# Kernel optimization log

Hardware: AMD Instinct MI355X
Metric: run time of the kernel (lower is better)

## Reference

```python
import jax, jax.numpy as jnp
import numpy as np

TAU = 0.5  # init tau
EPS = 1e-8  # F.cosine_similarity eps


def setup_inputs() -> dict:
    key = jax.random.key(0)
    k1, k2 = jax.random.split(key)
    N, D, NUM_CLASSES = 4096, 1024, 128
    layer_embeds = jax.random.normal(k1, (N, D), dtype=jnp.float32)
    y_true = jax.random.randint(k2, (N,), 0, NUM_CLASSES, dtype=jnp.int64)
    return {"layer_embeds": layer_embeds, "y_true": y_true}


def reference(layer_embeds, y_true):
    N = layer_embeds.shape[0]
    # batched cosine similarity, scaled like the original: (cos + 1) * 0.5 * tau
    norms = jnp.maximum(jnp.linalg.norm(layer_embeds, axis=1), EPS)  # [N]
    cos = (layer_embeds @ layer_embeds.T) / (norms[:, None] * norms[None, :])  # [N, N]
    S = (cos + 1.0) * 0.5 * TAU

    same = y_true[:, None] == y_true[None, :]  # [N, N]
    eye = jnp.eye(N, dtype=bool)
    pos_mask = same & ~eye            # same-label pairs, j != i
    neg_mask = ~same                  # different-label pairs (diag excluded since same there)

    # column 0: first positive (in j order), else stays 0
    has_pos = pos_mask.any(axis=1)
    first_pos = jnp.argmax(pos_mask, axis=1)
    pos_val = jnp.where(has_pos, S[jnp.arange(N), first_pos], 0.0)  # [N]

    # negatives fill columns 1.. in j order: col = 1 + (#negatives with j' < j)
    negi = neg_mask.astype(jnp.int32)
    col = 1 + jnp.cumsum(negi, axis=1) - negi  # [N, N]
    W = 2 * N  # pad one dummy column for non-negative entries
    cols = jnp.where(neg_mask, col, W - 1)
    rows = jnp.broadcast_to(jnp.arange(N)[:, None], (N, N))
    loss_temp = jnp.zeros((N, W), dtype=jnp.float32)
    loss_temp = loss_temp.at[rows, cols].set(jnp.where(neg_mask, S, 0.0))
    loss_temp = loss_temp.at[:, 0].set(pos_val)
    loss_temp = loss_temp[:, : 2 * N - 1]  # [N, 2N-1], matches torch buffer

    # -log_softmax, take column 0, sum over rows, divide by N
    lse = jax.nn.logsumexp(loss_temp, axis=1)  # [N]
    loss = jnp.sum(lse - loss_temp[:, 0]) / N
    return loss
```

## Files before the change

### kernel.cpp

```cpp
#include <hip/hip_runtime.h>
#include <hip/hip_bf16.h>
#include <math.h>

#define NN 4096
#define DD 1024
#define NCLS 128
#define TAU 0.5f
#define EPSV 1e-8f

typedef __bf16 bf16;
typedef __bf16 bf16x8 __attribute__((ext_vector_type(8)));
typedef __bf16 bf16x4 __attribute__((ext_vector_type(4)));
typedef float f32x4 __attribute__((ext_vector_type(4)));

__device__ __forceinline__ void gl2lds16(const void* g, void* l) {
    __builtin_amdgcn_global_load_lds(
        (const __attribute__((address_space(1))) void*)g,
        (__attribute__((address_space(3))) void*)l,
        16, 0, 0);
}

__global__ __launch_bounds__(256) void k_norm_cast(const float* __restrict__ X,
                                                   bf16* __restrict__ Xn,
                                                   float* __restrict__ rsum) {
    int w = threadIdx.x >> 6, lane = threadIdx.x & 63;
    int row = blockIdx.x * 4 + w;
    const float* xr = X + (size_t)row * DD;
    float4 v[4];
    float ss = 0.f;
#pragma unroll
    for (int c = 0; c < 4; ++c) {
        v[c] = *(const float4*)(xr + c * 256 + lane * 4);
        ss += v[c].x * v[c].x + v[c].y * v[c].y + v[c].z * v[c].z + v[c].w * v[c].w;
    }
#pragma unroll
    for (int m = 1; m < 64; m <<= 1) ss += __shfl_xor(ss, m, 64);
    float rn = 1.f / fmaxf(sqrtf(ss), EPSV);
    if (lane == 0) rsum[row] = 0.f;
#pragma unroll
    for (int c = 0; c < 4; ++c) {
        bf16x4 o;
        o.x = (bf16)(v[c].x * rn);
        o.y = (bf16)(v[c].y * rn);
        o.z = (bf16)(v[c].z * rn);
        o.w = (bf16)(v[c].w * rn);
        *(bf16x4*)(Xn + (size_t)row * DD + c * 256 + lane * 4) = o;
    }
}

__global__ __launch_bounds__(1024) void k_classes(const int* __restrict__ y,
                                                  int* __restrict__ cnt,
                                                  int* __restrict__ mn1,
                                                  int* __restrict__ mn2,
                                                  float* __restrict__ out) {
    __shared__ int sc[NCLS], s1[NCLS], s2[NCLS];
    int t = threadIdx.x;
    if (t < NCLS) { sc[t] = 0; s1[t] = 0x7fffffff; s2[t] = 0x7fffffff; }
    __syncthreads();
    int yv[4];
#pragma unroll
    for (int k = 0; k < 4; ++k) {
        int i = t + k * 1024;
        yv[k] = y[i];
        atomicAdd(&sc[yv[k]], 1);
        atomicMin(&s1[yv[k]], i);
    }
    __syncthreads();
#pragma unroll
    for (int k = 0; k < 4; ++k) {
        int i = t + k * 1024;
        if (s1[yv[k]] != i) atomicMin(&s2[yv[k]], i);
    }
    __syncthreads();
    if (t < NCLS) { cnt[t] = sc[t]; mn1[t] = s1[t]; mn2[t] = s2[t]; }
    if (t == 0) out[0] = 0.f;
}

__global__ __launch_bounds__(256) void k_gemm(const bf16* __restrict__ Xn,
                                              const int* __restrict__ y,
                                              float* __restrict__ rowsum) {
    __shared__ __align__(16) bf16 As[128 * 32];
    __shared__ __align__(16) bf16 Bs[128 * 32];
    __shared__ int yA[128], yB[128];

    int id = blockIdx.x;
    float ff = sqrtf((float)(8 * id + 1));
    int bj = (int)((ff - 1.f) * 0.5f);
    if (bj * (bj + 1) / 2 > id) bj--;
    if ((bj + 1) * (bj + 2) / 2 <= id) bj++;
    int bi = id - bj * (bj + 1) / 2;
    const int rowA0 = bi * 128;
    const int rowB0 = bj * 128;
    const bool diag = (bi == bj);

    const int tid = threadIdx.x;
    if (tid < 128) yA[tid] = y[rowA0 + tid];
    else           yB[tid - 128] = y[rowB0 + tid - 128];

    const int lane = tid & 63;
    const int w = tid >> 6;
    const int wm = w & 1, wn = w >> 1;
    const int lr = lane >> 4, lc = lane & 15;

    f32x4 acc[4][4];
#pragma unroll
    for (int i = 0; i < 4; ++i)
#pragma unroll
        for (int j = 0; j < 4; ++j) acc[i][j] = (f32x4){0.f, 0.f, 0.f, 0.f};

    const int r = tid >> 2;
    const int g = tid & 3;
    const int kg = g ^ ((r >> 1) & 3);
    const bf16* gA0 = Xn + (size_t)(rowA0 + r) * DD + kg * 8;
    const bf16* gA1 = gA0 + (size_t)64 * DD;
    const bf16* gB0 = Xn + (size_t)(rowB0 + r) * DD + kg * 8;
    const bf16* gB1 = gB0 + (size_t)64 * DD;
    bf16* lA0 = As + tid * 8;
    bf16* lA1 = As + 64 * 32 + tid * 8;
    bf16* lB0 = Bs + tid * 8;
    bf16* lB1 = Bs + 64 * 32 + tid * 8;

    const int sw = (lc >> 1) & 3;

    for (int k0 = 0; k0 < DD; k0 += 32) {
        __syncthreads();
        gl2lds16(gA0 + k0, lA0);
        gl2lds16(gA1 + k0, lA1);
        gl2lds16(gB0 + k0, lB0);
        gl2lds16(gB1 + k0, lB1);
        __syncthreads();

        bf16x8 af[4], bfr[4];
#pragma unroll
        for (int mt = 0; mt < 4; ++mt)
            af[mt] = *(const bf16x8*)(As + (wm * 64 + mt * 16 + lc) * 32 + ((lr ^ sw) * 8));
#pragma unroll
        for (int nt = 0; nt < 4; ++nt)
            bfr[nt] = *(const bf16x8*)(Bs + (wn * 64 + nt * 16 + lc) * 32 + ((lr ^ sw) * 8));
#pragma unroll
        for (int mt = 0; mt < 4; ++mt)
#pragma unroll
            for (int nt = 0; nt < 4; ++nt)
                acc[mt][nt] = __builtin_amdgcn_mfma_f32_16x16x32_bf16(
                    af[mt], bfr[nt], acc[mt][nt], 0, 0, 0);
    }

    int ycol[4];
#pragma unroll
    for (int nt = 0; nt < 4; ++nt) ycol[nt] = yB[wn * 64 + nt * 16 + lc];
    float colacc[4] = {0.f, 0.f, 0.f, 0.f};
#pragma unroll
    for (int mt = 0; mt < 4; ++mt) {
#pragma unroll
        for (int rr = 0; rr < 4; ++rr) {
            int rloc = wm * 64 + mt * 16 + lr * 4 + rr;
            int yrow = yA[rloc];
            float s = 0.f;
#pragma unroll
            for (int nt = 0; nt < 4; ++nt) {
                float Sv = (acc[mt][nt][rr] + 1.f) * (0.5f * TAU);
                float e = (ycol[nt] != yrow) ? __expf(Sv) : 0.f;
                s += e;
                colacc[nt] += e;
            }
            s += __shfl_xor(s, 1, 16);
            s += __shfl_xor(s, 2, 16);
            s += __shfl_xor(s, 4, 16);
            s += __shfl_xor(s, 8, 16);
            if (lc == 0) atomicAdd(&rowsum[rowA0 + rloc], s);
        }
    }
    if (!diag) {
#pragma unroll
        for (int nt = 0; nt < 4; ++nt) {
            float cs = colacc[nt];
            cs += __shfl_xor(cs, 16, 64);
            cs += __shfl_xor(cs, 32, 64);
            if (lane < 16) atomicAdd(&rowsum[rowB0 + wn * 64 + nt * 16 + lane], cs);
        }
    }
}

__global__ __launch_bounds__(256) void k_tail(const bf16* __restrict__ Xn,
                                              const int* __restrict__ y,
                                              const int* __restrict__ cnt,
                                              const int* __restrict__ mn1,
                                              const int* __restrict__ mn2,
                                              const float* __restrict__ rowsum,
                                              float* __restrict__ out) {
    int w = threadIdx.x >> 6, lane = threadIdx.x & 63;
    int i = blockIdx.x * 4 + w;
    int c = y[i];
    int cc = cnt[c];
    float pv = 0.f;
    if (cc >= 2) {
        int fp = (mn1[c] == i) ? mn2[c] : mn1[c];
        const bf16* xi = Xn + (size_t)i * DD;
        const bf16* xf = Xn + (size_t)fp * DD;
        float dot = 0.f;
#pragma unroll
        for (int q = 0; q < 2; ++q) {
            bf16x8 a = *(const bf16x8*)(xi + q * 512 + lane * 8);
            bf16x8 b = *(const bf16x8*)(xf + q * 512 + lane * 8);
#pragma unroll
            for (int e = 0; e < 8; ++e) dot += (float)a[e] * (float)b[e];
        }
#pragma unroll
        for (int m = 1; m < 64; m <<= 1) dot += __shfl_xor(dot, m, 64);
        pv = (dot + 1.f) * (0.5f * TAU);
    }
    float contrib = logf(rowsum[i] + __expf(pv) + (float)(NN - 2 + cc)) - pv;
    __shared__ float wsum[4];
    if (lane == 0) wsum[w] = contrib;
    __syncthreads();
    if (threadIdx.x == 0)
        atomicAdd(out, (wsum[0] + wsum[1] + wsum[2] + wsum[3]) * (1.f / (float)NN));
}

extern "C" void kernel_launch(void* const* d_in, const int* in_sizes, int n_in,
                              void* d_out, int out_size, void* d_ws, size_t ws_size,
                              hipStream_t stream) {
    const float* X = (const float*)d_in[0];
    const int* y = (const int*)d_in[1];
    float* out = (float*)d_out;

    char* ws = (char*)d_ws;
    bf16* Xn    = (bf16*)ws;
    float* rsum = (float*)(ws + 8 * 1024 * 1024);
    int* cnt    = (int*)(ws + 8 * 1024 * 1024 + 16 * 1024);
    int* mn1    = (int*)(ws + 8 * 1024 * 1024 + 16 * 1024 + 512);
    int* mn2    = (int*)(ws + 8 * 1024 * 1024 + 16 * 1024 + 1024);

    k_norm_cast<<<dim3(NN / 4), 256, 0, stream>>>(X, Xn, rsum);
    k_classes<<<dim3(1), 1024, 0, stream>>>(y, cnt, mn1, mn2, out);
    k_gemm<<<dim3(528), 256, 0, stream>>>(Xn, y, rsum);
    k_tail<<<dim3(NN / 4), 256, 0, stream>>>(Xn, y, cnt, mn1, mn2, rsum, out);
}
```

Measured before the change: 115.7 us.

## Double-buffer GEMM LDS tiles and fuse norm and class-stat kernels

New measurement: 119.9 us. 1.04x slower.

```diff
diff --git a/kernel.cpp b/kernel.cpp
--- a/kernel.cpp
+++ b/kernel.cpp
@@ -20,67 +20,68 @@
         16, 0, 0);
 }
 
-__global__ __launch_bounds__(256) void k_norm_cast(const float* __restrict__ X,
-                                                   bf16* __restrict__ Xn,
-                                                   float* __restrict__ rsum) {
-    int w = threadIdx.x >> 6, lane = threadIdx.x & 63;
-    int row = blockIdx.x * 4 + w;
-    const float* xr = X + (size_t)row * DD;
-    float4 v[4];
-    float ss = 0.f;
-#pragma unroll
-    for (int c = 0; c < 4; ++c) {
-        v[c] = *(const float4*)(xr + c * 256 + lane * 4);
-        ss += v[c].x * v[c].x + v[c].y * v[c].y + v[c].z * v[c].z + v[c].w * v[c].w;
-    }
-#pragma unroll
-    for (int m = 1; m < 64; m <<= 1) ss += __shfl_xor(ss, m, 64);
-    float rn = 1.f / fmaxf(sqrtf(ss), EPSV);
-    if (lane == 0) rsum[row] = 0.f;
-#pragma unroll
-    for (int c = 0; c < 4; ++c) {
-        bf16x4 o;
-        o.x = (bf16)(v[c].x * rn);
-        o.y = (bf16)(v[c].y * rn);
-        o.z = (bf16)(v[c].z * rn);
-        o.w = (bf16)(v[c].w * rn);
-        *(bf16x4*)(Xn + (size_t)row * DD + c * 256 + lane * 4) = o;
-    }
-}
-
-__global__ __launch_bounds__(1024) void k_classes(const int* __restrict__ y,
-                                                  int* __restrict__ cnt,
-                                                  int* __restrict__ mn1,
-                                                  int* __restrict__ mn2,
-                                                  float* __restrict__ out) {
-    __shared__ int sc[NCLS], s1[NCLS], s2[NCLS];
-    int t = threadIdx.x;
-    if (t < NCLS) { sc[t] = 0; s1[t] = 0x7fffffff; s2[t] = 0x7fffffff; }
-    __syncthreads();
-    int yv[4];
-#pragma unroll
-    for (int k = 0; k < 4; ++k) {
-        int i = t + k * 1024;
-        yv[k] = y[i];
-        atomicAdd(&sc[yv[k]], 1);
-        atomicMin(&s1[yv[k]], i);
-    }
-    __syncthreads();
-#pragma unroll
-    for (int k = 0; k < 4; ++k) {
-        int i = t + k * 1024;
-        if (s1[yv[k]] != i) atomicMin(&s2[yv[k]], i);
-    }
-    __syncthreads();
-    if (t < NCLS) { cnt[t] = sc[t]; mn1[t] = s1[t]; mn2[t] = s2[t]; }
-    if (t == 0) out[0] = 0.f;
+__global__ __launch_bounds__(256) void k_prep(const float* __restrict__ X,
+                                              bf16* __restrict__ Xn,
+                                              float* __restrict__ rsum,
+                                              const int* __restrict__ y,
+                                              int* __restrict__ cnt,
+                                              int* __restrict__ mn1,
+                                              int* __restrict__ mn2,
+                                              float* __restrict__ out) {
+    if (blockIdx.x < 1024) {
+        int w = threadIdx.x >> 6, lane = threadIdx.x & 63;
+        int row = blockIdx.x * 4 + w;
+        const float* xr = X + (size_t)row * DD;
+        float4 v[4];
+        float ss = 0.f;
+#pragma unroll
+        for (int c = 0; c < 4; ++c) {
+            v[c] = *(const float4*)(xr + c * 256 + lane * 4);
+            ss += v[c].x * v[c].x + v[c].y * v[c].y + v[c].z * v[c].z + v[c].w * v[c].w;
+        }
+#pragma unroll
+        for (int m = 1; m < 64; m <<= 1) ss += __shfl_xor(ss, m, 64);
+        float rn = 1.f / fmaxf(sqrtf(ss), EPSV);
+        if (lane == 0) rsum[row] = 0.f;
+#pragma unroll
+        for (int c = 0; c < 4; ++c) {
+            bf16x4 o;
+            o.x = (bf16)(v[c].x * rn);
+            o.y = (bf16)(v[c].y * rn);
+            o.z = (bf16)(v[c].z * rn);
+            o.w = (bf16)(v[c].w * rn);
+            *(bf16x4*)(Xn + (size_t)row * DD + c * 256 + lane * 4) = o;
+        }
+    } else {
+        __shared__ int sc[NCLS], s1[NCLS], s2[NCLS];
+        int t = threadIdx.x;
+        if (t < NCLS) { sc[t] = 0; s1[t] = 0x7fffffff; s2[t] = 0x7fffffff; }
+        __syncthreads();
+        int yv[16];
+#pragma unroll
+        for (int k = 0; k < 16; ++k) {
+            int i = k * 256 + t;
+            yv[k] = y[i];
+            atomicAdd(&sc[yv[k]], 1);
+            atomicMin(&s1[yv[k]], i);
+        }
+        __syncthreads();
+#pragma unroll
+        for (int k = 0; k < 16; ++k) {
+            int i = k * 256 + t;
+            if (s1[yv[k]] != i) atomicMin(&s2[yv[k]], i);
+        }
+        __syncthreads();
+        if (t < NCLS) { cnt[t] = sc[t]; mn1[t] = s1[t]; mn2[t] = s2[t]; }
+        if (t == 0) out[0] = 0.f;
+    }
 }
 
 __global__ __launch_bounds__(256) void k_gemm(const bf16* __restrict__ Xn,
                                               const int* __restrict__ y,
                                               float* __restrict__ rowsum) {
-    __shared__ __align__(16) bf16 As[128 * 32];
-    __shared__ __align__(16) bf16 Bs[128 * 32];
+    __shared__ __align__(16) bf16 As[2 * 128 * 32];
+    __shared__ __align__(16) bf16 Bs[2 * 128 * 32];
     __shared__ int yA[128], yB[128];
 
     int id = blockIdx.x;
@@ -121,22 +122,33 @@
     bf16* lB1 = Bs + 64 * 32 + tid * 8;
 
     const int sw = (lc >> 1) & 3;
-
-    for (int k0 = 0; k0 < DD; k0 += 32) {
-        __syncthreads();
-        gl2lds16(gA0 + k0, lA0);
-        gl2lds16(gA1 + k0, lA1);
-        gl2lds16(gB0 + k0, lB0);
-        gl2lds16(gB1 + k0, lB1);
-        __syncthreads();
-
+    const int slot8 = (lr ^ sw) * 8;
+
+    gl2lds16(gA0, lA0);
+    gl2lds16(gA1, lA1);
+    gl2lds16(gB0, lB0);
+    gl2lds16(gB1, lB1);
+
+    int s = 0;
+    for (int k0 = 0; k0 < DD; k0 += 32, s ^= 1) {
+        __syncthreads();
+        int nk = k0 + 32;
+        int noff = (s ^ 1) * 4096;
+        if (nk < DD) {
+            gl2lds16(gA0 + nk, lA0 + noff);
+            gl2lds16(gA1 + nk, lA1 + noff);
+            gl2lds16(gB0 + nk, lB0 + noff);
+            gl2lds16(gB1 + nk, lB1 + noff);
+        }
+        const bf16* Ab = As + s * 4096;
+        const bf16* Bb = Bs + s * 4096;
         bf16x8 af[4], bfr[4];
 #pragma unroll
         for (int mt = 0; mt < 4; ++mt)
-            af[mt] = *(const bf16x8*)(As + (wm * 64 + mt * 16 + lc) * 32 + ((lr ^ sw) * 8));
+            af[mt] = *(const bf16x8*)(Ab + (wm * 64 + mt * 16 + lc) * 32 + slot8);
 #pragma unroll
         for (int nt = 0; nt < 4; ++nt)
-            bfr[nt] = *(const bf16x8*)(Bs + (wn * 64 + nt * 16 + lc) * 32 + ((lr ^ sw) * 8));
+            bfr[nt] = *(const bf16x8*)(Bb + (wn * 64 + nt * 16 + lc) * 32 + slot8);
 #pragma unroll
         for (int mt = 0; mt < 4; ++mt)
 #pragma unroll
@@ -155,19 +167,19 @@
         for (int rr = 0; rr < 4; ++rr) {
             int rloc = wm * 64 + mt * 16 + lr * 4 + rr;
             int yrow = yA[rloc];
-            float s = 0.f;
+            float s2 = 0.f;
 #pragma unroll
             for (int nt = 0; nt < 4; ++nt) {
                 float Sv = (acc[mt][nt][rr] + 1.f) * (0.5f * TAU);
                 float e = (ycol[nt] != yrow) ? __expf(Sv) : 0.f;
-                s += e;
+                s2 += e;
                 colacc[nt] += e;
             }
-            s += __shfl_xor(s, 1, 16);
-            s += __shfl_xor(s, 2, 16);
-            s += __shfl_xor(s, 4, 16);
-            s += __shfl_xor(s, 8, 16);
-            if (lc == 0) atomicAdd(&rowsum[rowA0 + rloc], s);
+            s2 += __shfl_xor(s2, 1, 16);
+            s2 += __shfl_xor(s2, 2, 16);
+            s2 += __shfl_xor(s2, 4, 16);
+            s2 += __shfl_xor(s2, 8, 16);
+            if (lc == 0) atomicAdd(&rowsum[rowA0 + rloc], s2);
         }
     }
     if (!diag) {
@@ -231,8 +243,7 @@
     int* mn1    = (int*)(ws + 8 * 1024 * 1024 + 16 * 1024 + 512);
     int* mn2    = (int*)(ws + 8 * 1024 * 1024 + 16 * 1024 + 1024);
 
-    k_norm_cast<<<dim3(NN / 4), 256, 0, stream>>>(X, Xn, rsum);
-    k_classes<<<dim3(1), 1024, 0, stream>>>(y, cnt, mn1, mn2, out);
+    k_prep<<<dim3(1025), 256, 0, stream>>>(X, Xn, rsum, y, cnt, mn1, mn2, out);
     k_gemm<<<dim3(528), 256, 0, stream>>>(Xn, y, rsum);
     k_tail<<<dim3(NN / 4), 256, 0, stream>>>(Xn, y, cnt, mn1, mn2, rsum, out);
 }
```
